# Performance work log

Measured on AMD Instinct MI355X. Metric: run time of the kernel, lower is better.

## Reference

```python
import jax, jax.numpy as jnp
import numpy as np

N = 50000
IN, HID, OUT, HEADS = 128, 64, 64, 4


def seg_softmax(logits, seg, num):
    # softmax over edges grouped by destination node; logits [E, H]
    m = jax.ops.segment_max(logits, seg, num_segments=num)
    e = jnp.exp(logits - m[seg])
    s = jax.ops.segment_sum(e, seg, num_segments=num)
    return e / (s[seg] + 1e-16)


def gat_conv(x, src, dst, W, a_s, a_d, b, heads, concat):
    n = x.shape[0]
    h = (x @ W.T).reshape(n, heads, -1)           # [N, H, C]
    alpha_src = jnp.einsum('nhc,hc->nh', h, a_s)   # per-node src score
    alpha_dst = jnp.einsum('nhc,hc->nh', h, a_d)
    logits = jax.nn.leaky_relu(alpha_src[src] + alpha_dst[dst], 0.2)  # [E, H]
    alpha = seg_softmax(logits, dst, n)
    out = jax.ops.segment_sum(alpha[:, :, None] * h[src], dst, num_segments=n)  # [N, H, C]
    out = out.reshape(n, -1) if concat else out.mean(axis=1)
    return out + b


def setup_inputs():
    key = jax.random.key(0)
    ks = jax.random.split(key, 16)
    x = jax.random.normal(ks[0], (N, IN), dtype=jnp.float32)
    edge_index = jax.random.randint(ks[1], (2, 800000), 0, N, dtype=jnp.int64)

    def glorot(k, shape):
        fan = shape[-1]
        return jax.random.normal(k, shape, dtype=jnp.float32) / jnp.sqrt(jnp.float32(fan))

    d = {"x": x, "edge_index": edge_index}
    # layer 1: IN -> HID, HEADS heads, concat
    d["W1"] = glorot(ks[2], (HEADS * HID, IN))
    d["as1"] = glorot(ks[3], (HEADS, HID))
    d["ad1"] = glorot(ks[4], (HEADS, HID))
    d["b1"] = jnp.zeros((HEADS * HID,), jnp.float32)
    # layer 2: HID*HEADS -> HID, HEADS heads, concat
    d["W2"] = glorot(ks[5], (HEADS * HID, HEADS * HID))
    d["as2"] = glorot(ks[6], (HEADS, HID))
    d["ad2"] = glorot(ks[7], (HEADS, HID))
    d["b2"] = jnp.zeros((HEADS * HID,), jnp.float32)
    # layer 3: HID*HEADS -> OUT, 1 head
    d["W3"] = glorot(ks[8], (OUT, HEADS * HID))
    d["as3"] = glorot(ks[9], (1, OUT))
    d["ad3"] = glorot(ks[10], (1, OUT))
    d["b3"] = jnp.zeros((OUT,), jnp.float32)
    return d


def reference(x, edge_index, W1, as1, ad1, b1, W2, as2, ad2, b2, W3, as3, ad3, b3):
    # PyG GATConv adds self-loops by default
    loops = jnp.arange(N, dtype=edge_index.dtype)
    src = jnp.concatenate([edge_index[0], loops])
    dst = jnp.concatenate([edge_index[1], loops])

    h = jax.nn.relu(gat_conv(x, src, dst, W1, as1, ad1, b1, HEADS, True))
    h = jax.nn.relu(gat_conv(h, src, dst, W2, as2, ad2, b2, HEADS, True))
    out = gat_conv(h, src, dst, W3, as3, ad3, b3, 1, True)
    return out
```

## Files before the change

kernel.cpp:

```cpp
#include <hip/hip_runtime.h>
#include <hip/hip_bf16.h>
#include <math.h>


typedef __bf16 bf16x8 __attribute__((ext_vector_type(8)));
typedef float f32x4 __attribute__((ext_vector_type(4)));
typedef _Float16 half8v __attribute__((ext_vector_type(8)));

#define QINV 2048.0f
#define QDQ  4.8828125e-4f

__device__ __forceinline__ void gload_lds16(const void* g, void* l) {
  __builtin_amdgcn_global_load_lds(
      (const __attribute__((address_space(1))) unsigned int*)g,
      (__attribute__((address_space(3))) unsigned int*)l, 16, 0, 0);
}

__device__ __forceinline__ unsigned int splitf(float a) {
  __hip_bfloat16 h = __float2bfloat16(a);
  float hf = __bfloat162float(h);
  __hip_bfloat16 l = __float2bfloat16(a - hf);
  return (unsigned int)__builtin_bit_cast(unsigned short, h) |
         ((unsigned int)__builtin_bit_cast(unsigned short, l) << 16);
}

__device__ __forceinline__ float leaky02(float l) {
  return (l >= 0.f) ? l : 0.2f * l;
}

__device__ __forceinline__ short quant16(float v) {
  int q = (int)rintf(v * QINV);
  q = q > 32767 ? 32767 : (q < -32768 ? -32768 : q);
  return (short)q;
}


__global__ void init_counts_kernel(int* counts, int n) {
  int i = blockIdx.x * blockDim.x + threadIdx.x;
  if (i < n) counts[i] = 1;
}

__global__ void hist_kernel(const int* __restrict__ dst, int e, int* counts) {
  int i = blockIdx.x * blockDim.x + threadIdx.x;
  if (i < e) atomicAdd(&counts[dst[i]], 1);
}

__global__ __launch_bounds__(1024) void block_sum_kernel(const int* __restrict__ counts,
                                                         int* __restrict__ bsum, int n) {
  __shared__ int red[1024];
  int i = blockIdx.x * 1024 + threadIdx.x;
  red[threadIdx.x] = (i < n) ? counts[i] : 0;
  __syncthreads();
  #pragma unroll
  for (int off = 512; off > 0; off >>= 1) {
    if (threadIdx.x < off) red[threadIdx.x] += red[threadIdx.x + off];
    __syncthreads();
  }
  if (threadIdx.x == 0) bsum[blockIdx.x] = red[0];
}

__global__ void scan_sums_kernel(int* bsum, int nb) {
  int t = threadIdx.x;
  int c = (t < nb) ? bsum[t] : 0;
  int v = c;
  #pragma unroll
  for (int off = 1; off < 64; off <<= 1) {
    int u = __shfl_up(v, off);
    if (t >= off) v += u;
  }
  if (t < nb) bsum[t] = v - c;
}

__global__ __launch_bounds__(1024) void scan_final_kernel(const int* __restrict__ counts,
    const int* __restrict__ bsum, int* __restrict__ offsets, int* __restrict__ cursor, int n) {
  __shared__ int sc[1024];
  int i = blockIdx.x * 1024 + threadIdx.x;
  int c = (i < n) ? counts[i] : 0;
  sc[threadIdx.x] = c;
  __syncthreads();
  for (int off = 1; off < 1024; off <<= 1) {
    int v = 0;
    if (threadIdx.x >= off) v = sc[threadIdx.x - off];
    __syncthreads();
    sc[threadIdx.x] += v;
    __syncthreads();
  }
  int excl = sc[threadIdx.x] - c + bsum[blockIdx.x];
  if (i < n) {
    offsets[i] = excl;
    cursor[i] = excl;
  } else if (i == n) {
    offsets[n] = excl;
  }
}

__global__ void scatter_kernel(const int* __restrict__ src, const int* __restrict__ dst,
                               int e800, int etot, int* cursor, int* __restrict__ ssrc) {
  int i = blockIdx.x * blockDim.x + threadIdx.x;
  if (i >= etot) return;
  int s, d;
  if (i < e800) { s = src[i]; d = dst[i]; }
  else          { s = i - e800; d = s; }
  int pos = atomicAdd(&cursor[d], 1);
  ssrc[pos] = s;
}

__global__ void split_kernel(const float* __restrict__ in, uint4* __restrict__ out, int count4) {
  int i = blockIdx.x * blockDim.x + threadIdx.x;
  if (i >= count4) return;
  float4 v = reinterpret_cast<const float4*>(in)[i];
  uint4 o;
  o.x = splitf(v.x); o.y = splitf(v.y); o.z = splitf(v.z); o.w = splitf(v.w);
  out[i] = o;
}

__global__ void splitW_kernel(const float* __restrict__ W1, const float* __restrict__ W2,
                              const float* __restrict__ W3, uint4* __restrict__ o1,
                              uint4* __restrict__ o2, uint4* __restrict__ o3) {
  int i = blockIdx.x * blockDim.x + threadIdx.x;
  const float* in;
  uint4* out;
  int j;
  if (i < 8192)            { in = W1; out = o1; j = i; }
  else if (i < 8192+16384) { in = W2; out = o2; j = i - 8192; }
  else if (i < 8192+16384+4096) { in = W3; out = o3; j = i - (8192+16384); }
  else return;
  float4 v = reinterpret_cast<const float4*>(in)[j];
  uint4 o;
  o.x = splitf(v.x); o.y = splitf(v.y); o.z = splitf(v.z); o.w = splitf(v.w);
  out[j] = o;
}

template <int KP, int BM, int BN, int WAVES_M, int WAVES_N, int OTOT, int HEADS, bool FP16OUT>
__global__ __launch_bounds__(256) void gemm2_kernel(
    const unsigned short* __restrict__ A, const unsigned short* __restrict__ B,
    void* __restrict__ Cq, const float* __restrict__ a_s, const float* __restrict__ a_d,
    float* __restrict__ asrcO, float* __restrict__ adstO, int M) {
  constexpr int BK = 64;
  constexpr int NK = KP / BK;
  constexpr int MFRAG = BM / WAVES_M / 16;
  constexpr int NFRAG = BN / WAVES_N / 16;
  __shared__ unsigned short As[2][BM * BK];
  __shared__ unsigned short Bs[2][BN * BK];

  const int tid = threadIdx.x;
  const int lane = tid & 63;
  const int wid = tid >> 6;
  const int m0 = blockIdx.x * BM;
  const int o0 = blockIdx.y * BN;

  const int srow = tid >> 3;
  const int scolb = (tid & 7) * 16;
  const int sswz = (srow & 7) << 4;
  const char* aSrc = (const char*)A + (size_t)(m0 + srow) * (KP * 2) + (scolb ^ sswz);
  const char* bSrc = (const char*)B + (size_t)(o0 + srow) * (KP * 2) + (scolb ^ sswz);
  char* aDst0 = (char*)&As[0][0] + wid * 1024;
  char* bDst0 = (char*)&Bs[0][0] + wid * 1024;

  auto stage = [&](int buf, int kt) {
    const size_t ko = (size_t)kt * 128;
    char* ad = aDst0 + buf * (BM * 128);
    #pragma unroll
    for (int i = 0; i < BM / 32; ++i)
      gload_lds16(aSrc + ko + (size_t)i * 32 * (KP * 2), ad + i * 4096);
    char* bd = bDst0 + buf * (BN * 128);
    #pragma unroll
    for (int j = 0; j < BN / 32; ++j)
      gload_lds16(bSrc + ko + (size_t)j * 32 * (KP * 2), bd + j * 4096);
  };

  const int fr = lane & 15;
  const int fg = lane >> 4;
  const int fswz = (fr & 7) << 4;
  const int wm0 = (wid / WAVES_N) * (BM / WAVES_M);
  const int wn0 = (wid % WAVES_N) * (BN / WAVES_N);

  f32x4 acc[MFRAG][NFRAG];
  #pragma unroll
  for (int mi = 0; mi < MFRAG; ++mi)
    #pragma unroll
    for (int ni = 0; ni < NFRAG; ++ni) acc[mi][ni] = (f32x4)0.f;

  stage(0, 0);
  __syncthreads();

  for (int kt = 0; kt < NK; ++kt) {
    const int buf = kt & 1;
    if (kt + 1 < NK) stage(buf ^ 1, kt + 1);
    const char* asB = (const char*)&As[buf][0] + (wm0 + fr) * 128;
    const char* bsB = (const char*)&Bs[buf][0] + (wn0 + fr) * 128;
    #pragma unroll
    for (int kh = 0; kh < 2; ++kh) {
      const int kb = (kh * 64 + fg * 16) ^ fswz;
      bf16x8 af[MFRAG], bfr[NFRAG];
      #pragma unroll
      for (int mi = 0; mi < MFRAG; ++mi)
        af[mi] = *reinterpret_cast<const bf16x8*>(asB + mi * 16 * 128 + kb);
      #pragma unroll
      for (int ni = 0; ni < NFRAG; ++ni)
        bfr[ni] = *reinterpret_cast<const bf16x8*>(bsB + ni * 16 * 128 + kb);
      #pragma unroll
      for (int mi = 0; mi < MFRAG; ++mi)
        #pragma unroll
        for (int ni = 0; ni < NFRAG; ++ni)
          acc[mi][ni] = __builtin_amdgcn_mfma_f32_16x16x32_bf16(af[mi], bfr[ni], acc[mi][ni], 0, 0, 0);
    }
    __syncthreads();
  }

  const int head = (o0 + wn0) >> 6;
  float asl[NFRAG], adl[NFRAG];
  #pragma unroll
  for (int ni = 0; ni < NFRAG; ++ni) {
    int c64 = ni * 16 + fr;
    asl[ni] = a_s[head * 64 + c64];
    adl[ni] = a_d[head * 64 + c64];
  }
  #pragma unroll
  for (int mi = 0; mi < MFRAG; ++mi) {
    #pragma unroll
    for (int r = 0; r < 4; ++r) {
      int row = m0 + wm0 + mi * 16 + fg * 4 + r;
      float ps = 0.f, pd = 0.f;
      #pragma unroll
      for (int ni = 0; ni < NFRAG; ++ni) {
        ps = fmaf(acc[mi][ni][r], asl[ni], ps);
        pd = fmaf(acc[mi][ni][r], adl[ni], pd);
      }
      #pragma unroll
      for (int off = 1; off < 16; off <<= 1) {
        ps += __shfl_xor(ps, off);
        pd += __shfl_xor(pd, off);
      }
      if (row < M) {
        if (fr == 0) {
          asrcO[(size_t)row * HEADS + head] = ps;
          adstO[(size_t)row * HEADS + head] = pd;
        }
        #pragma unroll
        for (int ni = 0; ni < NFRAG; ++ni) {
          size_t ci = (size_t)row * OTOT + o0 + wn0 + ni * 16 + fr;
          if (FP16OUT) ((_Float16*)Cq)[ci] = (_Float16)acc[mi][ni][r];
          else         ((short*)Cq)[ci] = quant16(acc[mi][ni][r]);
        }
      }
    }
  }
}

__global__ __launch_bounds__(256) void aggregate4_kernel(
    const _Float16* __restrict__ hq, const float* __restrict__ asrc,
    const float* __restrict__ adst, const float* __restrict__ bias,
    const int* __restrict__ offsets, const int* __restrict__ ssrc,
    uint4* __restrict__ outp, int n) {
  int wid = threadIdx.x >> 6;
  int lane = threadIdx.x & 63;
  int sub = lane >> 5;
  int hl = lane & 31;
  int node = blockIdx.x * 8 + wid * 2 + sub;
  if (node >= n) return;
  int head = hl >> 3;
  int ch8 = hl * 8;
  float adv = adst[(size_t)node * 4 + head];
  int beg = offsets[node], end = offsets[node + 1];

  float s = 0.f;
  float A[8] = {};
  for (int e = beg; e < end; ++e) {
    int c = ssrc[e];
    float p = __expf(leaky02(asrc[(size_t)c * 4 + head] + adv));
    half8v hv = *reinterpret_cast<const half8v*>(&hq[(size_t)c * 256 + ch8]);
    s += p;
    #pragma unroll
    for (int j = 0; j < 8; ++j) A[j] = fmaf((float)hv[j], p, A[j]);
  }
  float inv = 1.f / (s + 1e-16f);
  float4 bv0 = *reinterpret_cast<const float4*>(&bias[ch8]);
  float4 bv1 = *reinterpret_cast<const float4*>(&bias[ch8 + 4]);
  float o[8];
  o[0] = fmaxf(A[0] * inv + bv0.x, 0.f);
  o[1] = fmaxf(A[1] * inv + bv0.y, 0.f);
  o[2] = fmaxf(A[2] * inv + bv0.z, 0.f);
  o[3] = fmaxf(A[3] * inv + bv0.w, 0.f);
  o[4] = fmaxf(A[4] * inv + bv1.x, 0.f);
  o[5] = fmaxf(A[5] * inv + bv1.y, 0.f);
  o[6] = fmaxf(A[6] * inv + bv1.z, 0.f);
  o[7] = fmaxf(A[7] * inv + bv1.w, 0.f);
  uint4 pk0, pk1;
  pk0.x = splitf(o[0]); pk0.y = splitf(o[1]); pk0.z = splitf(o[2]); pk0.w = splitf(o[3]);
  pk1.x = splitf(o[4]); pk1.y = splitf(o[5]); pk1.z = splitf(o[6]); pk1.w = splitf(o[7]);
  outp[(size_t)node * 64 + hl * 2 + 0] = pk0;
  outp[(size_t)node * 64 + hl * 2 + 1] = pk1;
}

__global__ __launch_bounds__(256) void aggregate1_kernel(
    const short* __restrict__ hq, const float* __restrict__ asrc,
    const float* __restrict__ adst, const float* __restrict__ bias,
    const int* __restrict__ offsets, const int* __restrict__ ssrc,
    float* __restrict__ out, int n) {
  int wid = threadIdx.x >> 6;
  int lane = threadIdx.x & 63;
  int node = blockIdx.x * 4 + wid;
  if (node >= n) return;
  int g = lane >> 4;
  int w = lane & 15;
  float adv = adst[node];
  int beg = offsets[node], end = offsets[node + 1];

  float s = 0.f;
  float4 A = {0, 0, 0, 0};
  int e0 = beg;
  for (; e0 + 3 < end; e0 += 4) {
    int src = ssrc[e0 + g];
    float p = __expf(leaky02(asrc[src] + adv));
    short4 q = *reinterpret_cast<const short4*>(&hq[(size_t)src * 64 + w * 4]);
    s += p;
    A.x += p * (float)q.x; A.y += p * (float)q.y;
    A.z += p * (float)q.z; A.w += p * (float)q.w;
  }
  if (e0 + g < end) {
    int src = ssrc[e0 + g];
    float p = __expf(leaky02(asrc[src] + adv));
    short4 q = *reinterpret_cast<const short4*>(&hq[(size_t)src * 64 + w * 4]);
    s += p;
    A.x += p * (float)q.x; A.y += p * (float)q.y;
    A.z += p * (float)q.z; A.w += p * (float)q.w;
  }
  #pragma unroll
  for (int off = 16; off < 64; off <<= 1) {
    s += __shfl_xor(s, off);
    A.x += __shfl_xor(A.x, off);
    A.y += __shfl_xor(A.y, off);
    A.z += __shfl_xor(A.z, off);
    A.w += __shfl_xor(A.w, off);
  }
  if (g == 0) {
    float inv = QDQ / (s + 1e-16f);
    float4 bv = *reinterpret_cast<const float4*>(&bias[w * 4]);
    float4 o;
    o.x = A.x * inv + bv.x;
    o.y = A.y * inv + bv.y;
    o.z = A.z * inv + bv.z;
    o.w = A.w * inv + bv.w;
    *reinterpret_cast<float4*>(&out[(size_t)node * 64 + w * 4]) = o;
  }
}


extern "C" void kernel_launch(void* const* d_in, const int* in_sizes, int n_in,
                              void* d_out, int out_size, void* d_ws, size_t ws_size,
                              hipStream_t stream) {
  const float* x   = (const float*)d_in[0];
  const int*   ei  = (const int*)d_in[1];
  const float* W1  = (const float*)d_in[2];
  const float* as1 = (const float*)d_in[3];
  const float* ad1 = (const float*)d_in[4];
  const float* b1  = (const float*)d_in[5];
  const float* W2  = (const float*)d_in[6];
  const float* as2 = (const float*)d_in[7];
  const float* ad2 = (const float*)d_in[8];
  const float* b2  = (const float*)d_in[9];
  const float* W3  = (const float*)d_in[10];
  const float* as3 = (const float*)d_in[11];
  const float* ad3 = (const float*)d_in[12];
  const float* b3  = (const float*)d_in[13];
  float* out = (float*)d_out;

  const int n    = in_sizes[0] / 128;
  const int e800 = in_sizes[1] / 2;
  const int etot = e800 + n;
  const int Mpad = 50048;

  char* ws = (char*)d_ws;
  size_t off = 0;
  auto alloc = [&](size_t bytes) -> void* {
    void* p = ws + off;
    off = (off + bytes + 255) & ~(size_t)255;
    return p;
  };
  void*           featQ  = alloc((size_t)Mpad * 256 * 2);
  unsigned short* hsplit = (unsigned short*)alloc((size_t)Mpad * 512 * 2);
  unsigned short* w1s    = (unsigned short*)alloc((size_t)256 * 256 * 2);
  unsigned short* w2s    = (unsigned short*)alloc((size_t)256 * 512 * 2);
  unsigned short* w3s    = (unsigned short*)alloc((size_t)64 * 512 * 2);
  float* asrc    = (float*)alloc((size_t)n * 4 * 4);
  float* adst    = (float*)alloc((size_t)n * 4 * 4);
  int*   ssrc    = (int*)alloc((size_t)etot * 4);
  int*   offsets = (int*)alloc((size_t)(n + 1) * 4);
  int*   cursor  = (int*)alloc((size_t)n * 4);
  int*   counts  = (int*)alloc((size_t)n * 4);
  int*   bsum    = (int*)alloc((size_t)64 * 4);

  const int* esrc = ei;
  const int* edst = ei + e800;
  const int nbScan = (n + 1024) / 1024;

  init_counts_kernel<<<(n + 255) / 256, 256, 0, stream>>>(counts, n);
  hist_kernel<<<(e800 + 255) / 256, 256, 0, stream>>>(edst, e800, counts);
  block_sum_kernel<<<nbScan, 1024, 0, stream>>>(counts, bsum, n);
  scan_sums_kernel<<<1, 64, 0, stream>>>(bsum, nbScan);
  scan_final_kernel<<<nbScan, 1024, 0, stream>>>(counts, bsum, offsets, cursor, n);
  scatter_kernel<<<(etot + 255) / 256, 256, 0, stream>>>(esrc, edst, e800, etot, cursor, ssrc);

  split_kernel<<<(n * 128 / 4 + 255) / 256, 256, 0, stream>>>(x, (uint4*)hsplit, n * 128 / 4);
  splitW_kernel<<<(8192 + 16384 + 4096 + 255) / 256, 256, 0, stream>>>(
      W1, W2, W3, (uint4*)w1s, (uint4*)w2s, (uint4*)w3s);

  const int mBlocks = Mpad / 128;

  gemm2_kernel<256, 128, 128, 2, 2, 256, 4, true><<<dim3(mBlocks, 2), 256, 0, stream>>>(
      hsplit, w1s, featQ, as1, ad1, asrc, adst, n);
  aggregate4_kernel<<<(n + 7) / 8, 256, 0, stream>>>(
      (const _Float16*)featQ, asrc, adst, b1, offsets, ssrc, (uint4*)hsplit, n);

  gemm2_kernel<512, 128, 128, 2, 2, 256, 4, true><<<dim3(mBlocks, 2), 256, 0, stream>>>(
      hsplit, w2s, featQ, as2, ad2, asrc, adst, n);
  aggregate4_kernel<<<(n + 7) / 8, 256, 0, stream>>>(
      (const _Float16*)featQ, asrc, adst, b2, offsets, ssrc, (uint4*)hsplit, n);

  gemm2_kernel<512, 128, 64, 4, 1, 64, 1, false><<<dim3(mBlocks, 1), 256, 0, stream>>>(
      hsplit, w3s, featQ, as3, ad3, asrc, adst, n);
  aggregate1_kernel<<<(n + 3) / 4, 256, 0, stream>>>(
      (const short*)featQ, asrc, adst, b3, offsets, ssrc, out, n);
}
```

Baseline: 374.5 us.

## Use fp16 GEMM inputs for layers 1-2 and head-major feature layout for aggregation

Layers 1 and 2 now convert inputs and weights to plain fp16 and use fp16 MFMA instead of the split bf16 hi/lo pair, which halves the GEMM K dimension and the staging traffic. GEMM outputs for these layers are written head-major, so each head's 64 channels are contiguous. Aggregation runs one grid slice per head, with 16 lanes per node, and unrolls the edge loop by four to keep more gathers in flight. Layer 3 keeps the split-bf16 path. Dropping the lo term costs input precision in the first two layers, and the padded unrolled loop reads past a node's edges using index 0.

```diff
diff --git a/kernel.cpp b/kernel.cpp
--- a/kernel.cpp
+++ b/kernel.cpp
@@ -6,7 +6,9 @@
 typedef __bf16 bf16x8 __attribute__((ext_vector_type(8)));
 typedef float f32x4 __attribute__((ext_vector_type(4)));
 typedef _Float16 half8v __attribute__((ext_vector_type(8)));
-
+typedef _Float16 half4v __attribute__((ext_vector_type(4)));
+
+#define MPAD 50048
 #define QINV 2048.0f
 #define QDQ  4.8828125e-4f
 
@@ -105,33 +107,38 @@
   ssrc[pos] = s;
 }
 
-__global__ void split_kernel(const float* __restrict__ in, uint4* __restrict__ out, int count4) {
+
+__global__ void cvtx_kernel(const float* __restrict__ in, _Float16* __restrict__ out, int count4) {
   int i = blockIdx.x * blockDim.x + threadIdx.x;
   if (i >= count4) return;
   float4 v = reinterpret_cast<const float4*>(in)[i];
-  uint4 o;
-  o.x = splitf(v.x); o.y = splitf(v.y); o.z = splitf(v.z); o.w = splitf(v.w);
-  out[i] = o;
-}
-
-__global__ void splitW_kernel(const float* __restrict__ W1, const float* __restrict__ W2,
-                              const float* __restrict__ W3, uint4* __restrict__ o1,
-                              uint4* __restrict__ o2, uint4* __restrict__ o3) {
+  half4v h = {(_Float16)v.x, (_Float16)v.y, (_Float16)v.z, (_Float16)v.w};
+  *reinterpret_cast<half4v*>(out + (size_t)i * 4) = h;
+}
+
+__global__ void cvtW_kernel(const float* __restrict__ W1, const float* __restrict__ W2,
+                            const float* __restrict__ W3, _Float16* __restrict__ o1,
+                            _Float16* __restrict__ o2, uint4* __restrict__ o3) {
   int i = blockIdx.x * blockDim.x + threadIdx.x;
-  const float* in;
-  uint4* out;
-  int j;
-  if (i < 8192)            { in = W1; out = o1; j = i; }
-  else if (i < 8192+16384) { in = W2; out = o2; j = i - 8192; }
-  else if (i < 8192+16384+4096) { in = W3; out = o3; j = i - (8192+16384); }
-  else return;
-  float4 v = reinterpret_cast<const float4*>(in)[j];
-  uint4 o;
-  o.x = splitf(v.x); o.y = splitf(v.y); o.z = splitf(v.z); o.w = splitf(v.w);
-  out[j] = o;
-}
-
-template <int KP, int BM, int BN, int WAVES_M, int WAVES_N, int OTOT, int HEADS, bool FP16OUT>
+  if (i < 8192) {
+    float4 v = reinterpret_cast<const float4*>(W1)[i];
+    half4v h = {(_Float16)v.x, (_Float16)v.y, (_Float16)v.z, (_Float16)v.w};
+    *reinterpret_cast<half4v*>(o1 + (size_t)i * 4) = h;
+  } else if (i < 8192 + 16384) {
+    int j = i - 8192;
+    float4 v = reinterpret_cast<const float4*>(W2)[j];
+    half4v h = {(_Float16)v.x, (_Float16)v.y, (_Float16)v.z, (_Float16)v.w};
+    *reinterpret_cast<half4v*>(o2 + (size_t)j * 4) = h;
+  } else if (i < 8192 + 16384 + 4096) {
+    int j = i - (8192 + 16384);
+    float4 v = reinterpret_cast<const float4*>(W3)[j];
+    uint4 o;
+    o.x = splitf(v.x); o.y = splitf(v.y); o.z = splitf(v.z); o.w = splitf(v.w);
+    o3[j] = o;
+  }
+}
+
+template <int KP, int BM, int BN, int WAVES_M, int WAVES_N, int HEADS, bool F16IN, bool HSPLIT>
 __global__ __launch_bounds__(256) void gemm2_kernel(
     const unsigned short* __restrict__ A, const unsigned short* __restrict__ B,
     void* __restrict__ Cq, const float* __restrict__ a_s, const float* __restrict__ a_d,
@@ -192,27 +199,42 @@
     #pragma unroll
     for (int kh = 0; kh < 2; ++kh) {
       const int kb = (kh * 64 + fg * 16) ^ fswz;
-      bf16x8 af[MFRAG], bfr[NFRAG];
-      #pragma unroll
-      for (int mi = 0; mi < MFRAG; ++mi)
-        af[mi] = *reinterpret_cast<const bf16x8*>(asB + mi * 16 * 128 + kb);
-      #pragma unroll
-      for (int ni = 0; ni < NFRAG; ++ni)
-        bfr[ni] = *reinterpret_cast<const bf16x8*>(bsB + ni * 16 * 128 + kb);
-      #pragma unroll
-      for (int mi = 0; mi < MFRAG; ++mi)
+      if constexpr (F16IN) {
+        half8v af[MFRAG], bfr[NFRAG];
+        #pragma unroll
+        for (int mi = 0; mi < MFRAG; ++mi)
+          af[mi] = *reinterpret_cast<const half8v*>(asB + mi * 16 * 128 + kb);
         #pragma unroll
         for (int ni = 0; ni < NFRAG; ++ni)
-          acc[mi][ni] = __builtin_amdgcn_mfma_f32_16x16x32_bf16(af[mi], bfr[ni], acc[mi][ni], 0, 0, 0);
+          bfr[ni] = *reinterpret_cast<const half8v*>(bsB + ni * 16 * 128 + kb);
+        #pragma unroll
+        for (int mi = 0; mi < MFRAG; ++mi)
+          #pragma unroll
+          for (int ni = 0; ni < NFRAG; ++ni)
+            acc[mi][ni] = __builtin_amdgcn_mfma_f32_16x16x32_f16(af[mi], bfr[ni], acc[mi][ni], 0, 0, 0);
+      } else {
+        bf16x8 af[MFRAG], bfr[NFRAG];
+        #pragma unroll
+        for (int mi = 0; mi < MFRAG; ++mi)
+          af[mi] = *reinterpret_cast<const bf16x8*>(asB + mi * 16 * 128 + kb);
+        #pragma unroll
+        for (int ni = 0; ni < NFRAG; ++ni)
+          bfr[ni] = *reinterpret_cast<const bf16x8*>(bsB + ni * 16 * 128 + kb);
+        #pragma unroll
+        for (int mi = 0; mi < MFRAG; ++mi)
+          #pragma unroll
+          for (int ni = 0; ni < NFRAG; ++ni)
+            acc[mi][ni] = __builtin_amdgcn_mfma_f32_16x16x32_bf16(af[mi], bfr[ni], acc[mi][ni], 0, 0, 0);
+      }
     }
     __syncthreads();
   }
 
-  const int head = (o0 + wn0) >> 6;
+  const int head = HSPLIT ? ((o0 + wn0) >> 6) : 0;
   float asl[NFRAG], adl[NFRAG];
   #pragma unroll
   for (int ni = 0; ni < NFRAG; ++ni) {
-    int c64 = ni * 16 + fr;
+    int c64 = HSPLIT ? (ni * 16 + fr) : (wn0 + ni * 16 + fr);
     asl[ni] = a_s[head * 64 + c64];
     adl[ni] = a_d[head * 64 + c64];
   }
@@ -239,58 +261,80 @@
         }
         #pragma unroll
         for (int ni = 0; ni < NFRAG; ++ni) {
-          size_t ci = (size_t)row * OTOT + o0 + wn0 + ni * 16 + fr;
-          if (FP16OUT) ((_Float16*)Cq)[ci] = (_Float16)acc[mi][ni][r];
-          else         ((short*)Cq)[ci] = quant16(acc[mi][ni][r]);
+          if constexpr (HSPLIT)
+            ((_Float16*)Cq)[(size_t)head * (MPAD * 64) + (size_t)row * 64 + ni * 16 + fr] =
+                (_Float16)acc[mi][ni][r];
+          else
+            ((short*)Cq)[(size_t)row * BN + wn0 + ni * 16 + fr] = quant16(acc[mi][ni][r]);
         }
       }
     }
   }
 }
 
+template <bool OUTBF>
 __global__ __launch_bounds__(256) void aggregate4_kernel(
-    const _Float16* __restrict__ hq, const float* __restrict__ asrc,
+    const _Float16* __restrict__ featH, const float* __restrict__ asrc,
     const float* __restrict__ adst, const float* __restrict__ bias,
     const int* __restrict__ offsets, const int* __restrict__ ssrc,
-    uint4* __restrict__ outp, int n) {
+    void* __restrict__ outp, int n) {
+  const int head = blockIdx.y;
+  const _Float16* fb = featH + (size_t)head * (MPAD * 64);
   int wid = threadIdx.x >> 6;
   int lane = threadIdx.x & 63;
-  int sub = lane >> 5;
-  int hl = lane & 31;
-  int node = blockIdx.x * 8 + wid * 2 + sub;
+  int node = blockIdx.x * 16 + wid * 4 + (lane >> 4);
   if (node >= n) return;
-  int head = hl >> 3;
-  int ch8 = hl * 8;
+  int c4 = (lane & 15) * 4;
   float adv = adst[(size_t)node * 4 + head];
   int beg = offsets[node], end = offsets[node + 1];
 
-  float s = 0.f;
-  float A[8] = {};
-  for (int e = beg; e < end; ++e) {
-    int c = ssrc[e];
-    float p = __expf(leaky02(asrc[(size_t)c * 4 + head] + adv));
-    half8v hv = *reinterpret_cast<const half8v*>(&hq[(size_t)c * 256 + ch8]);
-    s += p;
-    #pragma unroll
-    for (int j = 0; j < 8; ++j) A[j] = fmaf((float)hv[j], p, A[j]);
-  }
+  float s0 = 0.f, s1 = 0.f, s2 = 0.f, s3 = 0.f;
+  float4 A0 = {0,0,0,0}, A1 = {0,0,0,0}, A2 = {0,0,0,0}, A3 = {0,0,0,0};
+  for (int e = beg; e < end; e += 4) {
+    int c0 = ssrc[e + 0];
+    int c1 = (e + 1 < end) ? ssrc[e + 1] : 0;
+    int c2 = (e + 2 < end) ? ssrc[e + 2] : 0;
+    int c3 = (e + 3 < end) ? ssrc[e + 3] : 0;
+    float p0 = __expf(leaky02(asrc[(size_t)c0 * 4 + head] + adv));
+    float p1 = (e + 1 < end) ? __expf(leaky02(asrc[(size_t)c1 * 4 + head] + adv)) : 0.f;
+    float p2 = (e + 2 < end) ? __expf(leaky02(asrc[(size_t)c2 * 4 + head] + adv)) : 0.f;
+    float p3 = (e + 3 < end) ? __expf(leaky02(asrc[(size_t)c3 * 4 + head] + adv)) : 0.f;
+    half4v h0 = *reinterpret_cast<const half4v*>(fb + (size_t)c0 * 64 + c4);
+    half4v h1 = *reinterpret_cast<const half4v*>(fb + (size_t)c1 * 64 + c4);
+    half4v h2 = *reinterpret_cast<const half4v*>(fb + (size_t)c2 * 64 + c4);
+    half4v h3 = *reinterpret_cast<const half4v*>(fb + (size_t)c3 * 64 + c4);
+    s0 += p0; s1 += p1; s2 += p2; s3 += p3;
+    A0.x = fmaf((float)h0[0], p0, A0.x); A0.y = fmaf((float)h0[1], p0, A0.y);
+    A0.z = fmaf((float)h0[2], p0, A0.z); A0.w = fmaf((float)h0[3], p0, A0.w);
+    A1.x = fmaf((float)h1[0], p1, A1.x); A1.y = fmaf((float)h1[1], p1, A1.y);
+    A1.z = fmaf((float)h1[2], p1, A1.z); A1.w = fmaf((float)h1[3], p1, A1.w);
+    A2.x = fmaf((float)h2[0], p2, A2.x); A2.y = fmaf((float)h2[1], p2, A2.y);
+    A2.z = fmaf((float)h2[2], p2, A2.z); A2.w = fmaf((float)h2[3], p2, A2.w);
+    A3.x = fmaf((float)h3[0], p3, A3.x); A3.y = fmaf((float)h3[1], p3, A3.y);
+    A3.z = fmaf((float)h3[2], p3, A3.z); A3.w = fmaf((float)h3[3], p3, A3.w);
+  }
+  float s = (s0 + s1) + (s2 + s3);
+  float4 A;
+  A.x = (A0.x + A1.x) + (A2.x + A3.x);
+  A.y = (A0.y + A1.y) + (A2.y + A3.y);
+  A.z = (A0.z + A1.z) + (A2.z + A3.z);
+  A.w = (A0.w + A1.w) + (A2.w + A3.w);
+
   float inv = 1.f / (s + 1e-16f);
-  float4 bv0 = *reinterpret_cast<const float4*>(&bias[ch8]);
-  float4 bv1 = *reinterpret_cast<const float4*>(&bias[ch8 + 4]);
-  float o[8];
-  o[0] = fmaxf(A[0] * inv + bv0.x, 0.f);
-  o[1] = fmaxf(A[1] * inv + bv0.y, 0.f);
-  o[2] = fmaxf(A[2] * inv + bv0.z, 0.f);
-  o[3] = fmaxf(A[3] * inv + bv0.w, 0.f);
-  o[4] = fmaxf(A[4] * inv + bv1.x, 0.f);
-  o[5] = fmaxf(A[5] * inv + bv1.y, 0.f);
-  o[6] = fmaxf(A[6] * inv + bv1.z, 0.f);
-  o[7] = fmaxf(A[7] * inv + bv1.w, 0.f);
-  uint4 pk0, pk1;
-  pk0.x = splitf(o[0]); pk0.y = splitf(o[1]); pk0.z = splitf(o[2]); pk0.w = splitf(o[3]);
-  pk1.x = splitf(o[4]); pk1.y = splitf(o[5]); pk1.z = splitf(o[6]); pk1.w = splitf(o[7]);
-  outp[(size_t)node * 64 + hl * 2 + 0] = pk0;
-  outp[(size_t)node * 64 + hl * 2 + 1] = pk1;
+  float4 bv = *reinterpret_cast<const float4*>(&bias[head * 64 + c4]);
+  float4 o;
+  o.x = fmaxf(A.x * inv + bv.x, 0.f);
+  o.y = fmaxf(A.y * inv + bv.y, 0.f);
+  o.z = fmaxf(A.z * inv + bv.z, 0.f);
+  o.w = fmaxf(A.w * inv + bv.w, 0.f);
+  if (OUTBF) {
+    uint4 pk;
+    pk.x = splitf(o.x); pk.y = splitf(o.y); pk.z = splitf(o.z); pk.w = splitf(o.w);
+    reinterpret_cast<uint4*>(outp)[(size_t)node * 64 + head * 16 + (lane & 15)] = pk;
+  } else {
+    half4v hv = {(_Float16)o.x, (_Float16)o.y, (_Float16)o.z, (_Float16)o.w};
+    *reinterpret_cast<half4v*>((_Float16*)outp + (size_t)node * 256 + head * 64 + c4) = hv;
+  }
 }
 
 __global__ __launch_bounds__(256) void aggregate1_kernel(
@@ -369,7 +413,6 @@
   const int n    = in_sizes[0] / 128;
   const int e800 = in_sizes[1] / 2;
   const int etot = e800 + n;
-  const int Mpad = 50048;
 
   char* ws = (char*)d_ws;
   size_t off = 0;
@@ -378,14 +421,17 @@
     off = (off + bytes + 255) & ~(size_t)255;
     return p;
   };
-  void*           featQ  = alloc((size_t)Mpad * 256 * 2);
-  unsigned short* hsplit = (unsigned short*)alloc((size_t)Mpad * 512 * 2);
-  unsigned short* w1s    = (unsigned short*)alloc((size_t)256 * 256 * 2);
-  unsigned short* w2s    = (unsigned short*)alloc((size_t)256 * 512 * 2);
-  unsigned short* w3s    = (unsigned short*)alloc((size_t)64 * 512 * 2);
+  _Float16*       x16      = (_Float16*)alloc((size_t)MPAD * 128 * 2);
+  _Float16*       featH    = (_Float16*)alloc((size_t)4 * MPAD * 64 * 2);
+  short*          featL3   = (short*)alloc((size_t)MPAD * 64 * 2);
+  _Float16*       hsplit16 = (_Float16*)alloc((size_t)MPAD * 256 * 2);
+  unsigned short* hsplitBF = (unsigned short*)alloc((size_t)MPAD * 512 * 2);
+  _Float16*       w1f      = (_Float16*)alloc((size_t)256 * 128 * 2);
+  _Float16*       w2f      = (_Float16*)alloc((size_t)256 * 256 * 2);
+  unsigned short* w3s      = (unsigned short*)alloc((size_t)64 * 512 * 2);
   float* asrc    = (float*)alloc((size_t)n * 4 * 4);
   float* adst    = (float*)alloc((size_t)n * 4 * 4);
-  int*   ssrc    = (int*)alloc((size_t)etot * 4);
+  int*   ssrc    = (int*)alloc((size_t)(etot + 4) * 4);
   int*   offsets = (int*)alloc((size_t)(n + 1) * 4);
   int*   cursor  = (int*)alloc((size_t)n * 4);
   int*   counts  = (int*)alloc((size_t)n * 4);
@@ -402,24 +448,25 @@
   scan_final_kernel<<<nbScan, 1024, 0, stream>>>(counts, bsum, offsets, cursor, n);
   scatter_kernel<<<(etot + 255) / 256, 256, 0, stream>>>(esrc, edst, e800, etot, cursor, ssrc);
 
-  split_kernel<<<(n * 128 / 4 + 255) / 256, 256, 0, stream>>>(x, (uint4*)hsplit, n * 128 / 4);
-  splitW_kernel<<<(8192 + 16384 + 4096 + 255) / 256, 256, 0, stream>>>(
-      W1, W2, W3, (uint4*)w1s, (uint4*)w2s, (uint4*)w3s);
-
-  const int mBlocks = Mpad / 128;
-
-  gemm2_kernel<256, 128, 128, 2, 2, 256, 4, true><<<dim3(mBlocks, 2), 256, 0, stream>>>(
-      hsplit, w1s, featQ, as1, ad1, asrc, adst, n);
-  aggregate4_kernel<<<(n + 7) / 8, 256, 0, stream>>>(
-      (const _Float16*)featQ, asrc, adst, b1, offsets, ssrc, (uint4*)hsplit, n);
-
-  gemm2_kernel<512, 128, 128, 2, 2, 256, 4, true><<<dim3(mBlocks, 2), 256, 0, stream>>>(
-      hsplit, w2s, featQ, as2, ad2, asrc, adst, n);
-  aggregate4_kernel<<<(n + 7) / 8, 256, 0, stream>>>(
-      (const _Float16*)featQ, asrc, adst, b2, offsets, ssrc, (uint4*)hsplit, n);
-
-  gemm2_kernel<512, 128, 64, 4, 1, 64, 1, false><<<dim3(mBlocks, 1), 256, 0, stream>>>(
-      hsplit, w3s, featQ, as3, ad3, asrc, adst, n);
+  cvtx_kernel<<<(n * 128 / 4 + 255) / 256, 256, 0, stream>>>(x, x16, n * 128 / 4);
+  cvtW_kernel<<<(8192 + 16384 + 4096 + 255) / 256, 256, 0, stream>>>(
+      W1, W2, W3, w1f, w2f, (uint4*)w3s);
+
+  const int mBlocks = MPAD / 128;
+  const int aggBlocks = (n + 15) / 16;
+
+  gemm2_kernel<128, 128, 128, 2, 2, 4, true, true><<<dim3(mBlocks, 2), 256, 0, stream>>>(
+      (const unsigned short*)x16, (const unsigned short*)w1f, featH, as1, ad1, asrc, adst, n);
+  aggregate4_kernel<false><<<dim3(aggBlocks, 4), 256, 0, stream>>>(
+      featH, asrc, adst, b1, offsets, ssrc, hsplit16, n);
+
+  gemm2_kernel<256, 128, 128, 2, 2, 4, true, true><<<dim3(mBlocks, 2), 256, 0, stream>>>(
+      (const unsigned short*)hsplit16, (const unsigned short*)w2f, featH, as2, ad2, asrc, adst, n);
+  aggregate4_kernel<true><<<dim3(aggBlocks, 4), 256, 0, stream>>>(
+      featH, asrc, adst, b2, offsets, ssrc, hsplitBF, n);
+
+  gemm2_kernel<512, 128, 64, 4, 1, 1, false, false><<<dim3(mBlocks, 1), 256, 0, stream>>>(
+      hsplitBF, w3s, featL3, as3, ad3, asrc, adst, n);
   aggregate1_kernel<<<(n + 3) / 4, 256, 0, stream>>>(
-      (const short*)featQ, asrc, adst, b3, offsets, ssrc, out, n);
-}
+      featL3, asrc, adst, b3, offsets, ssrc, out, n);
+}
```

After: 405.8 us. 8.4% more time.
